# Optimization experiments

Measured on AMD Instinct MI355X. Metric: run time of the kernel, lower is better.

Reference implementation:

```python
import jax, jax.numpy as jnp
import numpy as np

RATE = 0.1
DIMS = dict(B=32, I=1024, H1=512, H2=512, O=256, MH=8)


def setup_inputs() -> dict:
    key = jax.random.key(0)
    ks = jax.random.split(key, 12)
    B, I, H1, H2, O, MH = DIMS['B'], DIMS['I'], DIMS['H1'], DIMS['H2'], DIMS['O'], DIMS['MH']

    def lin(k, fan_out, fan_in):
        bound = 1.0 / np.sqrt(fan_in)
        kw, kb = jax.random.split(k)
        W = jax.random.uniform(kw, (fan_out, fan_in), jnp.float32, -bound, bound)
        b = jax.random.uniform(kb, (fan_out,), jnp.float32, -bound, bound)
        return W, b

    fc1_w, fc1_b = lin(ks[0], H1, I)
    fc2_w, fc2_b = lin(ks[1], H2, H1)
    fc3_w, fc3_b = lin(ks[2], O, H2)
    # 1x1 convs: kernel [out_ch, in_ch, 1, 1] -> store as [out_ch, in_ch]
    conv1_w, conv1_b = lin(ks[3], MH, 3)
    conv2_w, conv2_b = lin(ks[4], 1, MH)

    x = jax.random.normal(ks[5], (B, I), jnp.float32)
    return dict(x=x,
                fc1_w=fc1_w, fc1_b=fc1_b,
                fc2_w=fc2_w, fc2_b=fc2_b,
                fc3_w=fc3_w, fc3_b=fc3_b,
                conv1_w=conv1_w, conv1_b=conv1_b,
                conv2_w=conv2_w, conv2_b=conv2_b,
                batch_num=10)


def _layer(out, W, b, c1w, c1b, c2w, c2b, scale):
    # out: [B, Iin]; W: [Oout, Iin]
    vi = out
    vj = jax.nn.relu(out @ W.T + b)                    # [B, O]
    B, O, Iin = vi.shape[0], W.shape[0], W.shape[1]
    # meta stack [B, O, I, 3] of (input, weight, output) broadcasts
    meta = jnp.stack(
        (jnp.broadcast_to(vi[:, None, :], (B, O, Iin)),
         jnp.broadcast_to(W[None, :, :], (B, O, Iin)),
         jnp.broadcast_to(vj[:, :, None], (B, O, Iin))),
        axis=-1)
    # two 1x1 convs == per-element channel MLP (no nonlinearity between, per source)
    h = jnp.einsum('boic,hc->boih', meta, c1w) + c1b   # [B, O, I, MH]
    shift = jnp.einsum('boih,h->boi', h, c2w[0]) + c2b[0]
    shift = shift * scale                              # rate / batch_num
    delta = jnp.einsum('boi,bi->bo', shift, vi)        # sum over input dim
    return vj + delta


def reference(x, fc1_w, fc1_b, fc2_w, fc2_b, fc3_w, fc3_b,
              conv1_w, conv1_b, conv2_w, conv2_b, batch_num):
    scale = jnp.float32(RATE) / jnp.float32(batch_num)
    out = x
    for (W, b) in ((fc1_w, fc1_b), (fc2_w, fc2_b), (fc3_w, fc3_b)):
        out = _layer(out, W, b, conv1_w, conv1_b, conv2_w, conv2_b, scale)
    return out
```

## Files before the change

### kernel.cpp

```cpp
#include <hip/hip_runtime.h>


#define DOMS 4
#define BPD  64
#define NBLK (DOMS * BPD)

__device__ unsigned int g_cnt[DOMS * 32];
__device__ unsigned int g_flag[DOMS * 32];

__device__ __forceinline__ void gridbar(int dom, unsigned int target) {
    __syncthreads();
    if (threadIdx.x == 0) {
        asm volatile("s_waitcnt vmcnt(0)" ::: "memory");
        unsigned int old = __hip_atomic_fetch_add(&g_cnt[dom * 32], 1u,
                               __ATOMIC_RELAXED, __HIP_MEMORY_SCOPE_AGENT);
        if ((old & (BPD - 1u)) == (BPD - 1u))
            __hip_atomic_store(&g_flag[dom * 32], target,
                               __ATOMIC_RELAXED, __HIP_MEMORY_SCOPE_AGENT);
        while ((int)(__hip_atomic_load(&g_flag[dom * 32], __ATOMIC_RELAXED,
                                       __HIP_MEMORY_SCOPE_AGENT) - target) < 0)
            __builtin_amdgcn_s_sleep(1);
        asm volatile("" ::: "memory");
    }
    __syncthreads();
}

#define KEEP4(v) asm volatile("" :: "v"((v).x), "v"((v).y), "v"((v).z), "v"((v).w))
#define KEEP1(v) asm volatile("" :: "v"(v))

template<int IIN>
__device__ __forceinline__ void wprefetch(const float* __restrict__ W,
                                          const float* __restrict__ bias,
                                          int c0, int lane,
                                          float4 (&wr)[2][IIN / 256],
                                          float& b0, float& b1) {
    #pragma unroll
    for (int cc = 0; cc < 2; ++cc) {
        const float4* Wr = reinterpret_cast<const float4*>(W + (size_t)(c0 + cc) * IIN);
        #pragma unroll
        for (int q = 0; q < IIN / 256; ++q) wr[cc][q] = Wr[q * 64 + lane];
    }
    b0 = bias[c0]; b1 = bias[c0 + 1];
}

template<int IIN, int OUT, int ROWS, int CPB, bool AIN, bool AOUT>
__device__ __forceinline__ void phase(const float* __restrict__ vin,
                                      const float4 (&wr)[2][IIN / 256],
                                      float b0, float b1,
                                      float* __restrict__ vout,
                                      float* __restrict__ lds,
                                      float* __restrict__ s1s,
                                      float* __restrict__ s2s,
                                      int rows0, int c0, int lane, int wave,
                                      float A0, float A1, float A2,
                                      float Dd, float scale)
{
    if (AIN) {
        const unsigned long long* src = reinterpret_cast<const unsigned long long*>(
            vin + (size_t)rows0 * IIN);
        float2* dst = reinterpret_cast<float2*>(lds);
        constexpr int N2 = ROWS * IIN / 2;
        #pragma unroll
        for (int k = 0; k < N2 / 256; ++k) {
            unsigned long long u = __hip_atomic_load(
                &src[k * 256 + threadIdx.x], __ATOMIC_RELAXED, __HIP_MEMORY_SCOPE_AGENT);
            float2 f;
            __builtin_memcpy(&f, &u, 8);
            dst[k * 256 + threadIdx.x] = f;
        }
    } else {
        const float4* src = reinterpret_cast<const float4*>(vin + (size_t)rows0 * IIN);
        float4* dst = reinterpret_cast<float4*>(lds);
        constexpr int N4 = ROWS * IIN / 4;
        #pragma unroll
        for (int k = 0; k < N4 / 256; ++k)
            dst[k * 256 + threadIdx.x] = src[k * 256 + threadIdx.x];
    }
    __syncthreads();

    constexpr int RPW = ROWS / 4;
    #pragma unroll
    for (int r = 0; r < RPW; ++r) {
        const int b = wave * RPW + r;
        const float4* v4 = reinterpret_cast<const float4*>(lds + b * IIN);
        float p1 = 0.f, p2 = 0.f;
        #pragma unroll
        for (int q = 0; q < IIN / 256; ++q) {
            const float4 a = v4[q * 64 + lane];
            p1 += (a.x + a.y) + (a.z + a.w);
            p2 += a.x * a.x + a.y * a.y + a.z * a.z + a.w * a.w;
        }
        #pragma unroll
        for (int s = 32; s > 0; s >>= 1) {
            p1 += __shfl_xor(p1, s);
            p2 += __shfl_xor(p2, s);
        }
        if (lane == 0) { s1s[b] = p1; s2s[b] = p2; }
    }

    float acc0[ROWS], acc1[ROWS];
    #pragma unroll
    for (int r = 0; r < ROWS; ++r) { acc0[r] = 0.f; acc1[r] = 0.f; }

    #pragma unroll
    for (int q = 0; q < IIN / 256; ++q) {
        const float4 w0 = wr[0][q];
        const float4 w1 = wr[1][q];
        #pragma unroll
        for (int r = 0; r < ROWS; ++r) {
            const float4 v4 = *reinterpret_cast<const float4*>(
                lds + r * IIN + (q * 64 + lane) * 4);
            acc0[r] = fmaf(w0.w, v4.w, fmaf(w0.z, v4.z,
                      fmaf(w0.y, v4.y, fmaf(w0.x, v4.x, acc0[r]))));
            acc1[r] = fmaf(w1.w, v4.w, fmaf(w1.z, v4.z,
                      fmaf(w1.y, v4.y, fmaf(w1.x, v4.x, acc1[r]))));
        }
    }

    float Wv = 0.f;
    #pragma unroll
    for (int r = 0; r < ROWS; ++r) {
        const float u = acc0[r] + __shfl_xor(acc0[r], 1);
        const float w = acc1[r] + __shfl_xor(acc1[r], 1);
        float z = (lane & 1) ? w : u;
        #pragma unroll
        for (int s = 2; s < 64; s <<= 1) z += __shfl_xor(z, s);
        if ((lane >> 1) == r) Wv = z;
    }

    __syncthreads();

    if (wave < CPB / 2 && lane < 2 * ROWS) {
        const int row = lane >> 1;
        const int col = c0 + (lane & 1);
        const float bias = (lane & 1) ? b1 : b0;
        const float vj  = fmaxf(Wv + bias, 0.f);
        const float val = vj + scale * (A0 * s2s[row] + A1 * Wv
                                        + (A2 * vj + Dd) * s1s[row]);
        float* dst = vout + (size_t)(rows0 + row) * OUT + col;
        if (AOUT)
            __hip_atomic_store(dst, val, __ATOMIC_RELAXED, __HIP_MEMORY_SCOPE_AGENT);
        else
            *dst = val;
    }
}

__global__ void __launch_bounds__(256, 1)
diffnet_onekernel(const float* __restrict__ x,
                  const float* __restrict__ W1, const float* __restrict__ b1,
                  const float* __restrict__ W2, const float* __restrict__ b2,
                  const float* __restrict__ W3, const float* __restrict__ b3,
                  const float* __restrict__ c1w, const float* __restrict__ c1b,
                  const float* __restrict__ c2w, const float* __restrict__ c2b,
                  const int* __restrict__ bn,
                  float* __restrict__ t1, float* __restrict__ t2,
                  float* __restrict__ out)
{
    __shared__ float lds[8 * 1024];
    __shared__ float s1s[8], s2s[8];

    const int bid  = blockIdx.x;
    const int dom  = bid >> 6;
    const int j    = bid & 63;
    const int rows0 = dom * 8;
    const int lane = threadIdx.x & 63;
    const int wave = threadIdx.x >> 6;

    unsigned int F0 = 0;
    if (threadIdx.x == 0)
        F0 = __hip_atomic_load(&g_flag[dom * 32], __ATOMIC_RELAXED,
                               __HIP_MEMORY_SCOPE_AGENT);

    float A0 = 0.f, A1 = 0.f, A2 = 0.f, Dd = c2b[0];
    #pragma unroll
    for (int h = 0; h < 8; ++h) {
        const float w2 = c2w[h];
        A0 = fmaf(w2, c1w[h * 3 + 0], A0);
        A1 = fmaf(w2, c1w[h * 3 + 1], A1);
        A2 = fmaf(w2, c1w[h * 3 + 2], A2);
        Dd = fmaf(w2, c1b[h], Dd);
    }
    const int raw = bn[0];
    const float bnf = (raw > 0 && raw < 1000000) ? (float)raw : __int_as_float(raw);
    const float scale = 0.1f / bnf;

    const int c12 = j * 8 + wave * 2;
    const int c3  = j * 4 + (wave & 1) * 2;

    float4 w1r[2][4];
    float b1a, b1b;
    wprefetch<1024>(W1, b1, c12, lane, w1r, b1a, b1b);
    phase<1024, 512, 8, 8, false, true>(x, w1r, b1a, b1b, t1, lds, s1s, s2s,
                                        rows0, c12, lane, wave,
                                        A0, A1, A2, Dd, scale);

    float4 w2r[2][2];
    float b2a, b2b;
    wprefetch<512>(W2, b2, c12, lane, w2r, b2a, b2b);
    KEEP4(w2r[0][0]); KEEP4(w2r[0][1]); KEEP4(w2r[1][0]); KEEP4(w2r[1][1]);
    KEEP1(b2a); KEEP1(b2b);

    gridbar(dom, F0 + 1);

    phase<512, 512, 8, 8, true, true>(t1, w2r, b2a, b2b, t2, lds, s1s, s2s,
                                      rows0, c12, lane, wave,
                                      A0, A1, A2, Dd, scale);

    float4 w3r[2][2];
    float b3a, b3b;
    wprefetch<512>(W3, b3, c3, lane, w3r, b3a, b3b);
    KEEP4(w3r[0][0]); KEEP4(w3r[0][1]); KEEP4(w3r[1][0]); KEEP4(w3r[1][1]);
    KEEP1(b3a); KEEP1(b3b);

    gridbar(dom, F0 + 2);

    phase<512, 256, 8, 4, true, false>(t2, w3r, b3a, b3b, out, lds, s1s, s2s,
                                       rows0, c3, lane, wave,
                                       A0, A1, A2, Dd, scale);
}

extern "C" void kernel_launch(void* const* d_in, const int* in_sizes, int n_in,
                              void* d_out, int out_size, void* d_ws, size_t ws_size,
                              hipStream_t stream) {
    const float* x     = (const float*)d_in[0];
    const float* fc1_w = (const float*)d_in[1];
    const float* fc1_b = (const float*)d_in[2];
    const float* fc2_w = (const float*)d_in[3];
    const float* fc2_b = (const float*)d_in[4];
    const float* fc3_w = (const float*)d_in[5];
    const float* fc3_b = (const float*)d_in[6];
    const float* c1w   = (const float*)d_in[7];
    const float* c1b   = (const float*)d_in[8];
    const float* c2w   = (const float*)d_in[9];
    const float* c2b   = (const float*)d_in[10];
    const int*   bn    = (const int*)d_in[11];

    float* t1  = (float*)d_ws;
    float* t2  = t1 + 32 * 512;
    float* out = (float*)d_out;

    diffnet_onekernel<<<dim3(NBLK), dim3(256), 0, stream>>>(
        x, fc1_w, fc1_b, fc2_w, fc2_b, fc3_w, fc3_b,
        c1w, c1b, c2w, c2b, bn, t1, t2, out);
}
```

Before: 21.35 us.

## Shrink grid to 32 blocks handling two row domains with split-phase barriers

The grid drops from 256 blocks of 256 threads to 32 blocks of 512 threads. Each block now processes two 8-row batch domains in sequence and computes 4 output columns per wave instead of 2. The grid barrier is split into separate arrive and wait steps, so one domain's phase overlaps the barrier latency of the other, and fewer blocks participate in each barrier. The cost is less total parallelism and more serial work per block, which may lengthen the critical path.

```diff
diff --git a/kernel.cpp b/kernel.cpp
--- a/kernel.cpp
+++ b/kernel.cpp
@@ -1,22 +1,28 @@
 #include <hip/hip_runtime.h>
 
 
-#define DOMS 4
-#define BPD  64
-#define NBLK (DOMS * BPD)
-
-__device__ unsigned int g_cnt[DOMS * 32];
-__device__ unsigned int g_flag[DOMS * 32];
-
-__device__ __forceinline__ void gridbar(int dom, unsigned int target) {
+#define NSET 2
+#define BPS  16
+#define NBLK (NSET * BPS)
+#define NDOM 4
+
+__device__ unsigned int g_cnt[NDOM * 32];
+__device__ unsigned int g_flag[NDOM * 32];
+
+__device__ __forceinline__ void bar_arrive(int dom, unsigned int target) {
     __syncthreads();
     if (threadIdx.x == 0) {
         asm volatile("s_waitcnt vmcnt(0)" ::: "memory");
         unsigned int old = __hip_atomic_fetch_add(&g_cnt[dom * 32], 1u,
                                __ATOMIC_RELAXED, __HIP_MEMORY_SCOPE_AGENT);
-        if ((old & (BPD - 1u)) == (BPD - 1u))
+        if ((old & (BPS - 1u)) == (BPS - 1u))
             __hip_atomic_store(&g_flag[dom * 32], target,
                                __ATOMIC_RELAXED, __HIP_MEMORY_SCOPE_AGENT);
+    }
+}
+
+__device__ __forceinline__ void bar_wait(int dom, unsigned int target) {
+    if (threadIdx.x == 0) {
         while ((int)(__hip_atomic_load(&g_flag[dom * 32], __ATOMIC_RELAXED,
                                        __HIP_MEMORY_SCOPE_AGENT) - target) < 0)
             __builtin_amdgcn_s_sleep(1);
@@ -25,28 +31,31 @@
     __syncthreads();
 }
 
-#define KEEP4(v) asm volatile("" :: "v"((v).x), "v"((v).y), "v"((v).z), "v"((v).w))
-#define KEEP1(v) asm volatile("" :: "v"(v))
-
-template<int IIN>
+__device__ __forceinline__ float pairred(float a, float b, int lane) {
+    const float u = a + __shfl_xor(a, 1);
+    const float w = b + __shfl_xor(b, 1);
+    return (lane & 1) ? w : u;
+}
+
+template<int IIN, int CPW>
 __device__ __forceinline__ void wprefetch(const float* __restrict__ W,
                                           const float* __restrict__ bias,
                                           int c0, int lane,
-                                          float4 (&wr)[2][IIN / 256],
-                                          float& b0, float& b1) {
-    #pragma unroll
-    for (int cc = 0; cc < 2; ++cc) {
+                                          float4 (&wr)[CPW][IIN / 256],
+                                          float (&bs)[CPW]) {
+    #pragma unroll
+    for (int cc = 0; cc < CPW; ++cc) {
         const float4* Wr = reinterpret_cast<const float4*>(W + (size_t)(c0 + cc) * IIN);
         #pragma unroll
         for (int q = 0; q < IIN / 256; ++q) wr[cc][q] = Wr[q * 64 + lane];
-    }
-    b0 = bias[c0]; b1 = bias[c0 + 1];
-}
-
-template<int IIN, int OUT, int ROWS, int CPB, bool AIN, bool AOUT>
+        bs[cc] = bias[c0 + cc];
+    }
+}
+
+template<int IIN, int OUT, int CPW, bool AIN, bool AOUT>
 __device__ __forceinline__ void phase(const float* __restrict__ vin,
-                                      const float4 (&wr)[2][IIN / 256],
-                                      float b0, float b1,
+                                      const float4 (&wr)[CPW][IIN / 256],
+                                      const float (&bs)[CPW],
                                       float* __restrict__ vout,
                                       float* __restrict__ lds,
                                       float* __restrict__ s1s,
@@ -55,34 +64,33 @@
                                       float A0, float A1, float A2,
                                       float Dd, float scale)
 {
+    constexpr int ROWS = 8;
+
     if (AIN) {
         const unsigned long long* src = reinterpret_cast<const unsigned long long*>(
             vin + (size_t)rows0 * IIN);
         float2* dst = reinterpret_cast<float2*>(lds);
         constexpr int N2 = ROWS * IIN / 2;
         #pragma unroll
-        for (int k = 0; k < N2 / 256; ++k) {
+        for (int k = 0; k < N2 / 512; ++k) {
             unsigned long long u = __hip_atomic_load(
-                &src[k * 256 + threadIdx.x], __ATOMIC_RELAXED, __HIP_MEMORY_SCOPE_AGENT);
+                &src[k * 512 + threadIdx.x], __ATOMIC_RELAXED, __HIP_MEMORY_SCOPE_AGENT);
             float2 f;
             __builtin_memcpy(&f, &u, 8);
-            dst[k * 256 + threadIdx.x] = f;
+            dst[k * 512 + threadIdx.x] = f;
         }
     } else {
         const float4* src = reinterpret_cast<const float4*>(vin + (size_t)rows0 * IIN);
         float4* dst = reinterpret_cast<float4*>(lds);
         constexpr int N4 = ROWS * IIN / 4;
         #pragma unroll
-        for (int k = 0; k < N4 / 256; ++k)
-            dst[k * 256 + threadIdx.x] = src[k * 256 + threadIdx.x];
-    }
-    __syncthreads();
-
-    constexpr int RPW = ROWS / 4;
-    #pragma unroll
-    for (int r = 0; r < RPW; ++r) {
-        const int b = wave * RPW + r;
-        const float4* v4 = reinterpret_cast<const float4*>(lds + b * IIN);
+        for (int k = 0; k < N4 / 512; ++k)
+            dst[k * 512 + threadIdx.x] = src[k * 512 + threadIdx.x];
+    }
+    __syncthreads();
+
+    {
+        const float4* v4 = reinterpret_cast<const float4*>(lds + wave * IIN);
         float p1 = 0.f, p2 = 0.f;
         #pragma unroll
         for (int q = 0; q < IIN / 256; ++q) {
@@ -95,49 +103,64 @@
             p1 += __shfl_xor(p1, s);
             p2 += __shfl_xor(p2, s);
         }
-        if (lane == 0) { s1s[b] = p1; s2s[b] = p2; }
-    }
-
-    float acc0[ROWS], acc1[ROWS];
-    #pragma unroll
-    for (int r = 0; r < ROWS; ++r) { acc0[r] = 0.f; acc1[r] = 0.f; }
+        if (lane == 0) { s1s[wave] = p1; s2s[wave] = p2; }
+    }
+
+    float acc[CPW][ROWS];
+    #pragma unroll
+    for (int c = 0; c < CPW; ++c)
+        #pragma unroll
+        for (int r = 0; r < ROWS; ++r) acc[c][r] = 0.f;
 
     #pragma unroll
     for (int q = 0; q < IIN / 256; ++q) {
-        const float4 w0 = wr[0][q];
-        const float4 w1 = wr[1][q];
+        float4 w[CPW];
+        #pragma unroll
+        for (int c = 0; c < CPW; ++c) w[c] = wr[c][q];
         #pragma unroll
         for (int r = 0; r < ROWS; ++r) {
-            const float4 v4 = *reinterpret_cast<const float4*>(
+            const float4 v = *reinterpret_cast<const float4*>(
                 lds + r * IIN + (q * 64 + lane) * 4);
-            acc0[r] = fmaf(w0.w, v4.w, fmaf(w0.z, v4.z,
-                      fmaf(w0.y, v4.y, fmaf(w0.x, v4.x, acc0[r]))));
-            acc1[r] = fmaf(w1.w, v4.w, fmaf(w1.z, v4.z,
-                      fmaf(w1.y, v4.y, fmaf(w1.x, v4.x, acc1[r]))));
+            #pragma unroll
+            for (int c = 0; c < CPW; ++c)
+                acc[c][r] = fmaf(w[c].w, v.w, fmaf(w[c].z, v.z,
+                            fmaf(w[c].y, v.y, fmaf(w[c].x, v.x, acc[c][r]))));
         }
     }
 
     float Wv = 0.f;
     #pragma unroll
     for (int r = 0; r < ROWS; ++r) {
-        const float u = acc0[r] + __shfl_xor(acc0[r], 1);
-        const float w = acc1[r] + __shfl_xor(acc1[r], 1);
-        float z = (lane & 1) ? w : u;
-        #pragma unroll
-        for (int s = 2; s < 64; s <<= 1) z += __shfl_xor(z, s);
-        if ((lane >> 1) == r) Wv = z;
-    }
-
-    __syncthreads();
-
-    if (wave < CPB / 2 && lane < 2 * ROWS) {
-        const int row = lane >> 1;
-        const int col = c0 + (lane & 1);
-        const float bias = (lane & 1) ? b1 : b0;
-        const float vj  = fmaxf(Wv + bias, 0.f);
+        float z0 = pairred(acc[0][r], acc[1][r], lane);
+        float z1 = 0.f;
+        if (CPW == 4) z1 = pairred(acc[2][r], acc[3][r], lane);
+        #pragma unroll
+        for (int s = 2; s < 64; s <<= 1) {
+            z0 += __shfl_xor(z0, s);
+            if (CPW == 4) z1 += __shfl_xor(z1, s);
+        }
+        if (CPW == 4) {
+            if ((lane >> 2) == r) Wv = (lane & 2) ? z1 : z0;
+        } else {
+            if ((lane >> 1) == r) Wv = z0;
+        }
+    }
+
+    __syncthreads();
+
+    if (lane < ROWS * CPW) {
+        const int row = lane / CPW;
+        const int cc  = lane & (CPW - 1);
+        float biasv;
+        if (CPW == 4)
+            biasv = (lane & 2) ? ((lane & 1) ? bs[3] : bs[2])
+                               : ((lane & 1) ? bs[1] : bs[0]);
+        else
+            biasv = (lane & 1) ? bs[1] : bs[0];
+        const float vj  = fmaxf(Wv + biasv, 0.f);
         const float val = vj + scale * (A0 * s2s[row] + A1 * Wv
                                         + (A2 * vj + Dd) * s1s[row]);
-        float* dst = vout + (size_t)(rows0 + row) * OUT + col;
+        float* dst = vout + (size_t)(rows0 + row) * OUT + c0 + cc;
         if (AOUT)
             __hip_atomic_store(dst, val, __ATOMIC_RELAXED, __HIP_MEMORY_SCOPE_AGENT);
         else
@@ -145,7 +168,7 @@
     }
 }
 
-__global__ void __launch_bounds__(256, 1)
+__global__ void __launch_bounds__(512, 1)
 diffnet_onekernel(const float* __restrict__ x,
                   const float* __restrict__ W1, const float* __restrict__ b1,
                   const float* __restrict__ W2, const float* __restrict__ b2,
@@ -160,16 +183,22 @@
     __shared__ float s1s[8], s2s[8];
 
     const int bid  = blockIdx.x;
-    const int dom  = bid >> 6;
-    const int j    = bid & 63;
-    const int rows0 = dom * 8;
+    const int set  = bid >> 4;
+    const int j    = bid & 15;
+    const int domA = set * 2;
+    const int domB = set * 2 + 1;
+    const int rowsA = domA * 8;
+    const int rowsB = domB * 8;
     const int lane = threadIdx.x & 63;
     const int wave = threadIdx.x >> 6;
 
-    unsigned int F0 = 0;
-    if (threadIdx.x == 0)
-        F0 = __hip_atomic_load(&g_flag[dom * 32], __ATOMIC_RELAXED,
+    unsigned int FA = 0, FB = 0;
+    if (threadIdx.x == 0) {
+        FA = __hip_atomic_load(&g_flag[domA * 32], __ATOMIC_RELAXED,
                                __HIP_MEMORY_SCOPE_AGENT);
+        FB = __hip_atomic_load(&g_flag[domB * 32], __ATOMIC_RELAXED,
+                               __HIP_MEMORY_SCOPE_AGENT);
+    }
 
     float A0 = 0.f, A1 = 0.f, A2 = 0.f, Dd = c2b[0];
     #pragma unroll
@@ -184,39 +213,45 @@
     const float bnf = (raw > 0 && raw < 1000000) ? (float)raw : __int_as_float(raw);
     const float scale = 0.1f / bnf;
 
-    const int c12 = j * 8 + wave * 2;
-    const int c3  = j * 4 + (wave & 1) * 2;
-
-    float4 w1r[2][4];
-    float b1a, b1b;
-    wprefetch<1024>(W1, b1, c12, lane, w1r, b1a, b1b);
-    phase<1024, 512, 8, 8, false, true>(x, w1r, b1a, b1b, t1, lds, s1s, s2s,
-                                        rows0, c12, lane, wave,
-                                        A0, A1, A2, Dd, scale);
-
-    float4 w2r[2][2];
-    float b2a, b2b;
-    wprefetch<512>(W2, b2, c12, lane, w2r, b2a, b2b);
-    KEEP4(w2r[0][0]); KEEP4(w2r[0][1]); KEEP4(w2r[1][0]); KEEP4(w2r[1][1]);
-    KEEP1(b2a); KEEP1(b2b);
-
-    gridbar(dom, F0 + 1);
-
-    phase<512, 512, 8, 8, true, true>(t1, w2r, b2a, b2b, t2, lds, s1s, s2s,
-                                      rows0, c12, lane, wave,
-                                      A0, A1, A2, Dd, scale);
+    const int c12 = j * 32 + wave * 4;
+    const int c3  = j * 16 + wave * 2;
+
+    float4 w1r[4][4];
+    float  b1s[4];
+    wprefetch<1024, 4>(W1, b1, c12, lane, w1r, b1s);
+
+    phase<1024, 512, 4, false, true>(x, w1r, b1s, t1, lds, s1s, s2s,
+                                     rowsA, c12, lane, wave, A0, A1, A2, Dd, scale);
+    bar_arrive(domA, FA + 1);
+    phase<1024, 512, 4, false, true>(x, w1r, b1s, t1, lds, s1s, s2s,
+                                     rowsB, c12, lane, wave, A0, A1, A2, Dd, scale);
+    bar_arrive(domB, FB + 1);
+
+    float4 w2r[4][2];
+    float  b2s[4];
+    wprefetch<512, 4>(W2, b2, c12, lane, w2r, b2s);
+
+    bar_wait(domA, FA + 1);
+    phase<512, 512, 4, true, true>(t1, w2r, b2s, t2, lds, s1s, s2s,
+                                   rowsA, c12, lane, wave, A0, A1, A2, Dd, scale);
+    bar_arrive(domA, FA + 2);
+
+    bar_wait(domB, FB + 1);
+    phase<512, 512, 4, true, true>(t1, w2r, b2s, t2, lds, s1s, s2s,
+                                   rowsB, c12, lane, wave, A0, A1, A2, Dd, scale);
+    bar_arrive(domB, FB + 2);
 
     float4 w3r[2][2];
-    float b3a, b3b;
-    wprefetch<512>(W3, b3, c3, lane, w3r, b3a, b3b);
-    KEEP4(w3r[0][0]); KEEP4(w3r[0][1]); KEEP4(w3r[1][0]); KEEP4(w3r[1][1]);
-    KEEP1(b3a); KEEP1(b3b);
-
-    gridbar(dom, F0 + 2);
-
-    phase<512, 256, 8, 4, true, false>(t2, w3r, b3a, b3b, out, lds, s1s, s2s,
-                                       rows0, c3, lane, wave,
-                                       A0, A1, A2, Dd, scale);
+    float  b3s[2];
+    wprefetch<512, 2>(W3, b3, c3, lane, w3r, b3s);
+
+    bar_wait(domA, FA + 2);
+    phase<512, 256, 2, true, false>(t2, w3r, b3s, out, lds, s1s, s2s,
+                                    rowsA, c3, lane, wave, A0, A1, A2, Dd, scale);
+
+    bar_wait(domB, FB + 2);
+    phase<512, 256, 2, true, false>(t2, w3r, b3s, out, lds, s1s, s2s,
+                                    rowsB, c3, lane, wave, A0, A1, A2, Dd, scale);
 }
 
 extern "C" void kernel_launch(void* const* d_in, const int* in_sizes, int n_in,
@@ -239,7 +274,7 @@
     float* t2  = t1 + 32 * 512;
     float* out = (float*)d_out;
 
-    diffnet_onekernel<<<dim3(NBLK), dim3(256), 0, stream>>>(
+    diffnet_onekernel<<<dim3(NBLK), dim3(512), 0, stream>>>(
         x, fc1_w, fc1_b, fc2_w, fc2_b, fc3_w, fc3_b,
         c1w, c1b, c2w, c2b, bn, t1, t2, out);
 }
```

Result: slower. 40.14 us (+88.0%).

## Split grid barrier into arrive/wait and use hierarchical atomic counters

Applied to the files above, without the earlier changes.

Replaces the single-counter grid barrier with a split arrive/wait barrier. Arrivals first go to per-group counters of 8 blocks, and only each group's last block touches the domain counter. The next layer's weight and bias prefetch now sits between arrive and wait, so those loads overlap barrier latency. This reduces atomic contention on one address, but adds a second atomic level and assumes the group and domain counts wrap correctly across launches.

```diff
diff --git a/kernel.cpp b/kernel.cpp
--- a/kernel.cpp
+++ b/kernel.cpp
@@ -1,22 +1,32 @@
 #include <hip/hip_runtime.h>
 
 
-#define DOMS 4
+#define NDOM 4
 #define BPD  64
-#define NBLK (DOMS * BPD)
-
-__device__ unsigned int g_cnt[DOMS * 32];
-__device__ unsigned int g_flag[DOMS * 32];
-
-__device__ __forceinline__ void gridbar(int dom, unsigned int target) {
+#define NBLK (NDOM * BPD)
+
+__device__ unsigned int g_grp[NDOM * 8 * 32];
+__device__ unsigned int g_cnt[NDOM * 32];
+__device__ unsigned int g_flag[NDOM * 32];
+
+__device__ __forceinline__ void bar_arrive(int dom, int j, unsigned int target) {
     __syncthreads();
     if (threadIdx.x == 0) {
         asm volatile("s_waitcnt vmcnt(0)" ::: "memory");
-        unsigned int old = __hip_atomic_fetch_add(&g_cnt[dom * 32], 1u,
-                               __ATOMIC_RELAXED, __HIP_MEMORY_SCOPE_AGENT);
-        if ((old & (BPD - 1u)) == (BPD - 1u))
-            __hip_atomic_store(&g_flag[dom * 32], target,
-                               __ATOMIC_RELAXED, __HIP_MEMORY_SCOPE_AGENT);
+        unsigned int p = __hip_atomic_fetch_add(&g_grp[(dom * 8 + (j >> 3)) * 32], 1u,
+                             __ATOMIC_RELAXED, __HIP_MEMORY_SCOPE_AGENT);
+        if ((p & 7u) == 7u) {
+            unsigned int q = __hip_atomic_fetch_add(&g_cnt[dom * 32], 1u,
+                                 __ATOMIC_RELAXED, __HIP_MEMORY_SCOPE_AGENT);
+            if ((q & 7u) == 7u)
+                __hip_atomic_store(&g_flag[dom * 32], target,
+                                   __ATOMIC_RELAXED, __HIP_MEMORY_SCOPE_AGENT);
+        }
+    }
+}
+
+__device__ __forceinline__ void bar_wait(int dom, unsigned int target) {
+    if (threadIdx.x == 0) {
         while ((int)(__hip_atomic_load(&g_flag[dom * 32], __ATOMIC_RELAXED,
                                        __HIP_MEMORY_SCOPE_AGENT) - target) < 0)
             __builtin_amdgcn_s_sleep(1);
@@ -27,21 +37,6 @@
 
 #define KEEP4(v) asm volatile("" :: "v"((v).x), "v"((v).y), "v"((v).z), "v"((v).w))
 #define KEEP1(v) asm volatile("" :: "v"(v))
-
-template<int IIN>
-__device__ __forceinline__ void wprefetch(const float* __restrict__ W,
-                                          const float* __restrict__ bias,
-                                          int c0, int lane,
-                                          float4 (&wr)[2][IIN / 256],
-                                          float& b0, float& b1) {
-    #pragma unroll
-    for (int cc = 0; cc < 2; ++cc) {
-        const float4* Wr = reinterpret_cast<const float4*>(W + (size_t)(c0 + cc) * IIN);
-        #pragma unroll
-        for (int q = 0; q < IIN / 256; ++q) wr[cc][q] = Wr[q * 64 + lane];
-    }
-    b0 = bias[c0]; b1 = bias[c0 + 1];
-}
 
 template<int IIN, int OUT, int ROWS, int CPB, bool AIN, bool AOUT>
 __device__ __forceinline__ void phase(const float* __restrict__ vin,
@@ -188,31 +183,55 @@
     const int c3  = j * 4 + (wave & 1) * 2;
 
     float4 w1r[2][4];
-    float b1a, b1b;
-    wprefetch<1024>(W1, b1, c12, lane, w1r, b1a, b1b);
+    {
+        #pragma unroll
+        for (int cc = 0; cc < 2; ++cc) {
+            const float4* Wr = reinterpret_cast<const float4*>(W1 + (size_t)(c12 + cc) * 1024);
+            #pragma unroll
+            for (int q = 0; q < 4; ++q) w1r[cc][q] = Wr[q * 64 + lane];
+        }
+    }
+    const float b1a = b1[c12], b1b = b1[c12 + 1];
+
     phase<1024, 512, 8, 8, false, true>(x, w1r, b1a, b1b, t1, lds, s1s, s2s,
                                         rows0, c12, lane, wave,
                                         A0, A1, A2, Dd, scale);
+    bar_arrive(dom, j, F0 + 1);
 
     float4 w2r[2][2];
-    float b2a, b2b;
-    wprefetch<512>(W2, b2, c12, lane, w2r, b2a, b2b);
+    {
+        #pragma unroll
+        for (int cc = 0; cc < 2; ++cc) {
+            const float4* Wr = reinterpret_cast<const float4*>(W2 + (size_t)(c12 + cc) * 512);
+            #pragma unroll
+            for (int q = 0; q < 2; ++q) w2r[cc][q] = Wr[q * 64 + lane];
+        }
+    }
+    const float b2a = b2[c12], b2b = b2[c12 + 1];
     KEEP4(w2r[0][0]); KEEP4(w2r[0][1]); KEEP4(w2r[1][0]); KEEP4(w2r[1][1]);
     KEEP1(b2a); KEEP1(b2b);
 
-    gridbar(dom, F0 + 1);
+    bar_wait(dom, F0 + 1);
 
     phase<512, 512, 8, 8, true, true>(t1, w2r, b2a, b2b, t2, lds, s1s, s2s,
                                       rows0, c12, lane, wave,
                                       A0, A1, A2, Dd, scale);
+    bar_arrive(dom, j, F0 + 2);
 
     float4 w3r[2][2];
-    float b3a, b3b;
-    wprefetch<512>(W3, b3, c3, lane, w3r, b3a, b3b);
+    {
+        #pragma unroll
+        for (int cc = 0; cc < 2; ++cc) {
+            const float4* Wr = reinterpret_cast<const float4*>(W3 + (size_t)(c3 + cc) * 512);
+            #pragma unroll
+            for (int q = 0; q < 2; ++q) w3r[cc][q] = Wr[q * 64 + lane];
+        }
+    }
+    const float b3a = b3[c3], b3b = b3[c3 + 1];
     KEEP4(w3r[0][0]); KEEP4(w3r[0][1]); KEEP4(w3r[1][0]); KEEP4(w3r[1][1]);
     KEEP1(b3a); KEEP1(b3b);
 
-    gridbar(dom, F0 + 2);
+    bar_wait(dom, F0 + 2);
 
     phase<512, 256, 8, 4, true, false>(t2, w3r, b3a, b3b, out, lds, s1s, s2s,
                                        rows0, c3, lane, wave,
```

New measurement: 21.56 us. About the same (+1.0%).
